# Kernel tuning notes

Hardware: AMD Instinct MI355X
Metric: run time of the kernel (lower is better)

The kernel has to match this reference:

```python
import jax, jax.numpy as jnp
import numpy as np

B, T, F = 256, 2000, 42
H_VAD, H_NOISE, H_DEN = 24, 48, 96

def _gru_params(key, in_dim, hid):
    k1, k2, k3, k4 = jax.random.split(key, 4)
    s = 1.0 / np.sqrt(hid)
    return (jax.random.uniform(k1, (3 * hid, in_dim), jnp.float32, -s, s),
            jax.random.uniform(k2, (3 * hid, hid), jnp.float32, -s, s),
            jax.random.uniform(k3, (3 * hid,), jnp.float32, -s, s),
            jax.random.uniform(k4, (3 * hid,), jnp.float32, -s, s))

def setup_inputs() -> dict:
    key = jax.random.key(0)
    ks = jax.random.split(key, 12)
    x = jax.random.normal(ks[0], (B, T, F), jnp.float32)
    sd = 1.0 / np.sqrt(F)
    dense_w = jax.random.uniform(ks[1], (24, F), jnp.float32, -sd, sd)
    dense_b = jax.random.uniform(ks[2], (24,), jnp.float32, -sd, sd)
    vad_w_ih, vad_w_hh, vad_b_ih, vad_b_hh = _gru_params(ks[3], 24, H_VAD)
    sv = 1.0 / np.sqrt(H_VAD)
    vad_out_w = jax.random.uniform(ks[4], (1, H_VAD), jnp.float32, -sv, sv)
    vad_out_b = jax.random.uniform(ks[5], (1,), jnp.float32, -sv, sv)
    noise_w_ih, noise_w_hh, noise_b_ih, noise_b_hh = _gru_params(ks[6], F + 24 + H_VAD, H_NOISE)
    den_w_ih, den_w_hh, den_b_ih, den_b_hh = _gru_params(ks[7], F + H_VAD + H_NOISE, H_DEN)
    so = 1.0 / np.sqrt(H_DEN)
    out_w = jax.random.uniform(ks[8], (22, H_DEN), jnp.float32, -so, so)
    out_b = jax.random.uniform(ks[9], (22,), jnp.float32, -so, so)
    return dict(x=x, dense_w=dense_w, dense_b=dense_b,
                vad_w_ih=vad_w_ih, vad_w_hh=vad_w_hh, vad_b_ih=vad_b_ih, vad_b_hh=vad_b_hh,
                vad_out_w=vad_out_w, vad_out_b=vad_out_b,
                noise_w_ih=noise_w_ih, noise_w_hh=noise_w_hh, noise_b_ih=noise_b_ih, noise_b_hh=noise_b_hh,
                den_w_ih=den_w_ih, den_w_hh=den_w_hh, den_b_ih=den_b_ih, den_b_hh=den_b_hh,
                out_w=out_w, out_b=out_b)

def _gru(x_seq, w_ih, w_hh, b_ih, b_hh):
    # PyTorch GRU semantics, batch_first. x_seq: [B,T,I] -> hidden seq [B,T,H]
    hid = w_hh.shape[1]
    gx = jnp.einsum('bti,gi->btg', x_seq, w_ih) + b_ih  # precompute input gates [B,T,3H]
    h0 = jnp.zeros((x_seq.shape[0], hid), x_seq.dtype)
    def step(h, gx_t):
        gh = h @ w_hh.T + b_hh
        xr, xz, xn = jnp.split(gx_t, 3, axis=-1)
        hr, hz, hn = jnp.split(gh, 3, axis=-1)
        r = jax.nn.sigmoid(xr + hr)
        z = jax.nn.sigmoid(xz + hz)
        n = jnp.tanh(xn + r * hn)
        h_new = (1.0 - z) * n + z * h
        return h_new, h_new
    _, hs = jax.lax.scan(step, h0, jnp.swapaxes(gx, 0, 1))  # hs: [T,B,H]
    return jnp.swapaxes(hs, 0, 1)

def reference(x, dense_w, dense_b, vad_w_ih, vad_w_hh, vad_b_ih, vad_b_hh,
              vad_out_w, vad_out_b, noise_w_ih, noise_w_hh, noise_b_ih, noise_b_hh,
              den_w_ih, den_w_hh, den_b_ih, den_b_hh, out_w, out_b):
    tmp = jnp.tanh(jnp.einsum('btf,of->bto', x, dense_w) + dense_b)
    vad_gru = _gru(tmp, vad_w_ih, vad_w_hh, vad_b_ih, vad_b_hh)
    vad_out = jax.nn.sigmoid(jnp.einsum('bth,oh->bto', vad_gru, vad_out_w) + vad_out_b)
    noise_in = jnp.concatenate([tmp, vad_gru, x], axis=-1)
    noise_gru = _gru(noise_in, noise_w_ih, noise_w_hh, noise_b_ih, noise_b_hh)
    den_in = jnp.concatenate([vad_gru, jax.nn.relu(noise_gru), x], axis=-1)
    den_gru = _gru(den_in, den_w_ih, den_w_hh, den_b_ih, den_b_hh)
    den_out = jax.nn.sigmoid(jnp.einsum('bth,oh->bto', jax.nn.relu(den_gru), out_w) + out_b)
    return (den_out, vad_out)
```

## Files before the change

### kernel.cpp

```cpp
#include <hip/hip_runtime.h>
#include <hip/hip_bf16.h>

#define BB 256
#define TT 2000
#define FF 42
#define NTHREADS 640

__device__ __forceinline__ float bf2f(__hip_bfloat16 v) { return __bfloat162float(v); }
__device__ __forceinline__ float sig(float x) { return 1.0f / (1.0f + __expf(-x)); }
__device__ __forceinline__ float tanh_fast(float x) {
    float e = __expf(2.0f * x);
    return 1.0f - 2.0f / (e + 1.0f);
}
__device__ __forceinline__ float unpk_lo(unsigned u) {
    union { unsigned u; float f; } c; c.u = u << 16; return c.f;
}
__device__ __forceinline__ float unpk_hi(unsigned u) {
    union { unsigned u; float f; } c; c.u = u & 0xffff0000u; return c.f;
}
__device__ __forceinline__ unsigned f2bfbits(float f) {
    union { float f; unsigned u; } c; c.f = f;
    unsigned r = c.u + 0x7FFFu + ((c.u >> 16) & 1u);
    return r >> 16;
}
__device__ __forceinline__ unsigned pack2(float a, float b) {
    return f2bfbits(a) | (f2bfbits(b) << 16);
}
__device__ __forceinline__ float gld(const void* p, int i, bool f32) {
    return f32 ? ((const float*)p)[i] : bf2f(((const __hip_bfloat16*)p)[i]);
}

template<int NW>
__device__ __forceinline__ float dot_w2(const unsigned* __restrict__ w,
                                        const float* __restrict__ in, float acc) {
    const float2* in2 = (const float2*)in;
    float a0 = acc, a1 = 0.f;
    #pragma unroll
    for (int i = 0; i < NW; ++i) {
        unsigned u = w[i];
        float2 d = in2[i];
        a0 = fmaf(unpk_lo(u), d.x, a0);
        a1 = fmaf(unpk_hi(u), d.y, a1);
    }
    return a0 + a1;
}
template<int NW>
__device__ __forceinline__ float dot_reg2(const unsigned (&w)[57],
                                          const float* __restrict__ in, float acc) {
    const float2* in2 = (const float2*)in;
    float a0 = acc, a1 = 0.f;
    #pragma unroll
    for (int i = 0; i < NW; ++i) {
        unsigned u = w[i];
        float2 d = in2[i];
        a0 = fmaf(unpk_lo(u), d.x, a0);
        a1 = fmaf(unpk_hi(u), d.y, a1);
    }
    return a0 + a1;
}

__device__ void load_rows(unsigned* dst, const void* src, int O, int Kw, int K, int S,
                          int tid, int nt, bool f32) {
    for (int i = tid; i < O * Kw; i += nt) {
        int o = i / Kw, kp = i - o * Kw;
        dst[o * S + kp] = pack2(gld(src, o * K + 2 * kp, f32),
                                gld(src, o * K + 2 * kp + 1, f32));
    }
}
__device__ void load_V(float* dst, const void* src, int n, int tid, int nt, bool f32) {
    for (int i = tid; i < n; i += nt) dst[i] = gld(src, i, f32);
}

__global__ __launch_bounds__(NTHREADS, 1)
void rnn_fused(const void* __restrict__ x,
               const void* __restrict__ dense_w, const void* __restrict__ dense_b,
               const void* __restrict__ vad_w_ih, const void* __restrict__ vad_w_hh,
               const void* __restrict__ vad_b_ih, const void* __restrict__ vad_b_hh,
               const void* __restrict__ vad_out_w, const void* __restrict__ vad_out_b,
               const void* __restrict__ noise_w_ih, const void* __restrict__ noise_w_hh,
               const void* __restrict__ noise_b_ih, const void* __restrict__ noise_b_hh,
               const void* __restrict__ den_w_ih, const void* __restrict__ den_w_hh,
               const void* __restrict__ den_b_ih, const void* __restrict__ den_b_hh,
               const void* __restrict__ out_w, const void* __restrict__ out_b,
               void* __restrict__ d_out) {
    __shared__ __align__(16) unsigned sDWp[24 * 21];
    __shared__ __align__(16) unsigned sVIHp[72 * 13];
    __shared__ __align__(16) unsigned sVHHp[72 * 13];
    __shared__ __align__(16) unsigned sNIHp[144 * 45];
    __shared__ __align__(16) unsigned sNHHp[144 * 25];
    __shared__ __align__(16) unsigned sOWp[22 * 49];
    __shared__ unsigned sVOWp[12];
    __shared__ float sDB[24], sVBI[72], sVBH[72], sNBI[144], sNBH[144], sOB[22], sVOB[1];
    __shared__ __align__(16) float sXT[44];
    __shared__ __align__(16) float sTMP[24];
    __shared__ __align__(16) float sHV[24];
    __shared__ __align__(16) float sHN[48];
    __shared__ __align__(16) float sHD[96];
    __shared__ __align__(16) float sHR[96];
    __shared__ __align__(16) float sNIN[92];
    __shared__ __align__(16) float sDIN[116];
    __shared__ float sVPI[72], sVPH[72];
    __shared__ float sNPI[144], sNPH[144];
    __shared__ float sGI[288], sGH[288];
    __shared__ int sBad;

    const int tid = threadIdx.x;
    const int b = blockIdx.x;
    const int nt = NTHREADS;

    if (tid == 0) sBad = 0;
    __syncthreads();
    {
        const unsigned* w = (const unsigned*)dense_w;
        for (int i = tid; i < 500; i += nt) {
            float av = fabsf(unpk_lo(w[i]));
            if (!(av <= 1e3f)) { atomicAdd(&sBad, 1); break; }
        }
    }
    __syncthreads();
    const bool F32 = (sBad > 0);

    const float* xbf = (const float*)x + (size_t)b * TT * FF;
    const __hip_bfloat16* xbh = (const __hip_bfloat16*)x + (size_t)b * TT * FF;
    float* odf = (float*)d_out;
    __hip_bfloat16* odh = (__hip_bfloat16*)d_out;
    float* ovf = odf + (size_t)BB * TT * 22;
    __hip_bfloat16* ovh = odh + (size_t)BB * TT * 22;

    load_rows(sDWp,  dense_w,    24, 21, 42, 21, tid, nt, F32);
    load_rows(sVIHp, vad_w_ih,   72, 12, 24, 13, tid, nt, F32);
    load_rows(sVHHp, vad_w_hh,   72, 12, 24, 13, tid, nt, F32);
    load_rows(sNIHp, noise_w_ih, 144, 45, 90, 45, tid, nt, F32);
    load_rows(sNHHp, noise_w_hh, 144, 24, 48, 25, tid, nt, F32);
    load_rows(sOWp,  out_w,      22, 48, 96, 49, tid, nt, F32);
    if (tid < 12) sVOWp[tid] = pack2(gld(vad_out_w, 2 * tid, F32),
                                     gld(vad_out_w, 2 * tid + 1, F32));
    load_V(sDB,  dense_b,    24, tid, nt, F32);
    load_V(sVBI, vad_b_ih,   72, tid, nt, F32);
    load_V(sVBH, vad_b_hh,   72, tid, nt, F32);
    load_V(sNBI, noise_b_ih, 144, tid, nt, F32);
    load_V(sNBH, noise_b_hh, 144, tid, nt, F32);
    load_V(sOB,  out_b,      22, tid, nt, F32);
    if (tid == 0) sVOB[0] = gld(vad_out_b, 0, F32);

    unsigned wden[57];
    float bDen = 0.f;
    if (tid < 288) {
        #pragma unroll
        for (int i = 0; i < 57; ++i)
            wden[i] = pack2(gld(den_w_ih, tid * 114 + 2 * i, F32),
                            gld(den_w_ih, tid * 114 + 2 * i + 1, F32));
        bDen = gld(den_b_ih, tid, F32);
    } else if (tid >= 320 && tid < 608) {
        int o = tid - 320;
        #pragma unroll
        for (int i = 0; i < 48; ++i)
            wden[i] = pack2(gld(den_w_hh, o * 96 + 2 * i, F32),
                            gld(den_w_hh, o * 96 + 2 * i + 1, F32));
        #pragma unroll
        for (int i = 48; i < 57; ++i) wden[i] = 0u;
        bDen = gld(den_b_hh, o, F32);
    } else {
        #pragma unroll
        for (int i = 0; i < 57; ++i) wden[i] = 0u;
    }

    for (int i = tid; i < 24; i += nt) { sHV[i] = 0.f; sTMP[i] = 0.f; }
    for (int i = tid; i < 48; i += nt) sHN[i] = 0.f;
    for (int i = tid; i < 96; i += nt) { sHD[i] = 0.f; sHR[i] = 0.f; }
    if (tid < 2) { sXT[42 + tid] = 0.f; sNIN[90 + tid] = 0.f; sDIN[114 + tid] = 0.f; }
    float xreg = 0.f;
    if (tid >= 128 && tid < 128 + FF) {
        int j = tid - 128;
        float v = F32 ? xbf[j] : bf2f(xbh[j]);
        sXT[j] = v;
        sNIN[48 + j] = v;
        sDIN[72 + j] = v;
        xreg = F32 ? xbf[FF + j] : bf2f(xbh[FF + j]);
    }
    __syncthreads();

    for (int t = 0; t < TT; ++t) {
        if (tid < 24) {
            float v = tanh_fast(dot_w2<21>(sDWp + tid * 21, sXT, sDB[tid]));
            sTMP[tid] = v;
            sNIN[tid] = v;
        } else if (tid >= 64 && tid < 86) {
            if (t > 0) {
                int o = tid - 64;
                float a = dot_w2<48>(sOWp + o * 49, sHR, sOB[o]);
                size_t oi = ((size_t)b * TT + (t - 1)) * 22 + o;
                float v = sig(a);
                if (F32) odf[oi] = v; else odh[oi] = __float2bfloat16(v);
            }
        }
        __syncthreads();

        if (tid < 72) {
            sVPI[tid] = dot_w2<12>(sVIHp + tid * 13, sTMP, sVBI[tid]);
        } else if (tid >= 128 && tid < 200) {
            int o = tid - 128;
            sVPH[o] = dot_w2<12>(sVHHp + o * 13, sHV, sVBH[o]);
        }
        __syncthreads();

        if (tid < 24) {
            float r = sig(sVPI[tid] + sVPH[tid]);
            float z = sig(sVPI[24 + tid] + sVPH[24 + tid]);
            float n = tanh_fast(sVPI[48 + tid] + r * sVPH[48 + tid]);
            float h = (1.f - z) * n + z * sHV[tid];
            sHV[tid] = h;
            sNIN[24 + tid] = h;
            sDIN[tid] = h;
        }
        __syncthreads();

        if (tid < 144) {
            sNPI[tid] = dot_w2<45>(sNIHp + tid * 45, sNIN, sNBI[tid]);
        } else if (tid >= 192 && tid < 336) {
            int o = tid - 192;
            sNPH[o] = dot_w2<24>(sNHHp + o * 25, sHN, sNBH[o]);
        }
        __syncthreads();

        if (tid < 48) {
            float r = sig(sNPI[tid] + sNPH[tid]);
            float z = sig(sNPI[48 + tid] + sNPH[48 + tid]);
            float n = tanh_fast(sNPI[96 + tid] + r * sNPH[96 + tid]);
            float h = (1.f - z) * n + z * sHN[tid];
            sHN[tid] = h;
            sDIN[24 + tid] = fmaxf(h, 0.f);
        }
        __syncthreads();

        if (tid < 288) {
            sGI[tid] = dot_reg2<57>(wden, sDIN, bDen);
        } else if (tid >= 320 && tid < 608) {
            sGH[tid - 320] = dot_reg2<48>(wden, sHD, bDen);
        }
        __syncthreads();

        if (tid < 96) {
            float r = sig(sGI[tid] + sGH[tid]);
            float z = sig(sGI[96 + tid] + sGH[96 + tid]);
            float n = tanh_fast(sGI[192 + tid] + r * sGH[192 + tid]);
            float h = (1.f - z) * n + z * sHD[tid];
            sHD[tid] = h;
            sHR[tid] = fmaxf(h, 0.f);
        } else if (tid >= 128 && tid < 128 + FF) {
            if (t + 1 < TT) {
                int j = tid - 128;
                sXT[j] = xreg;
                sNIN[48 + j] = xreg;
                sDIN[72 + j] = xreg;
                int t2 = (t + 2 < TT) ? (t + 2) : (TT - 1);
                xreg = F32 ? xbf[t2 * FF + j] : bf2f(xbh[t2 * FF + j]);
            }
        } else if (tid == 200) {
            float a = sVOB[0];
            const float2* hv2 = (const float2*)sHV;
            #pragma unroll
            for (int i = 0; i < 12; ++i) {
                unsigned u = sVOWp[i];
                float2 d = hv2[i];
                a = fmaf(unpk_lo(u), d.x, a);
                a = fmaf(unpk_hi(u), d.y, a);
            }
            size_t oi = (size_t)b * TT + t;
            float v = sig(a);
            if (F32) ovf[oi] = v; else ovh[oi] = __float2bfloat16(v);
        }
        __syncthreads();
    }

    if (tid >= 64 && tid < 86) {
        int o = tid - 64;
        float a = dot_w2<48>(sOWp + o * 49, sHR, sOB[o]);
        size_t oi = ((size_t)b * TT + (TT - 1)) * 22 + o;
        float v = sig(a);
        if (F32) odf[oi] = v; else odh[oi] = __float2bfloat16(v);
    }
}

extern "C" void kernel_launch(void* const* d_in, const int* in_sizes, int n_in,
                              void* d_out, int out_size, void* d_ws, size_t ws_size,
                              hipStream_t stream) {
    hipLaunchKernelGGL(rnn_fused, dim3(BB), dim3(NTHREADS), 0, stream,
                       d_in[0], d_in[1], d_in[2],
                       d_in[3], d_in[4], d_in[5], d_in[6],
                       d_in[7], d_in[8],
                       d_in[9], d_in[10], d_in[11], d_in[12],
                       d_in[13], d_in[14], d_in[15], d_in[16],
                       d_in[17], d_in[18], d_out);
}
```

Before: 10.04 ms.

## Restructure per-step schedule to cut barriers and overlap GRU stages

Reorganizes the per-timestep pipeline. The VAD GRU is fused into one 24-thread stage that computes all six gate dots and the update without a separate barrier. The dense-layer tanh for the next step and the den hidden-hidden matvec are moved into earlier stages so they overlap other work, and biases are held in registers instead of shared memory. The goal is fewer __syncthreads per step along the sequential critical path. In exchange, each VAD thread now does six dot products serially, and the x-staging logic is more intricate, so there is a risk of ordering bugs.

```diff
diff --git a/kernel.cpp b/kernel.cpp
--- a/kernel.cpp
+++ b/kernel.cpp
@@ -29,6 +29,7 @@
 __device__ __forceinline__ float gld(const void* p, int i, bool f32) {
     return f32 ? ((const float*)p)[i] : bf2f(((const __hip_bfloat16*)p)[i]);
 }
+
 
 template<int NW>
 __device__ __forceinline__ float dot_w2(const unsigned* __restrict__ w,
@@ -66,9 +67,6 @@
         dst[o * S + kp] = pack2(gld(src, o * K + 2 * kp, f32),
                                 gld(src, o * K + 2 * kp + 1, f32));
     }
-}
-__device__ void load_V(float* dst, const void* src, int n, int tid, int nt, bool f32) {
-    for (int i = tid; i < n; i += nt) dst[i] = gld(src, i, f32);
 }
 
 __global__ __launch_bounds__(NTHREADS, 1)
@@ -90,7 +88,6 @@
     __shared__ __align__(16) unsigned sNHHp[144 * 25];
     __shared__ __align__(16) unsigned sOWp[22 * 49];
     __shared__ unsigned sVOWp[12];
-    __shared__ float sDB[24], sVBI[72], sVBH[72], sNBI[144], sNBH[144], sOB[22], sVOB[1];
     __shared__ __align__(16) float sXT[44];
     __shared__ __align__(16) float sTMP[24];
     __shared__ __align__(16) float sHV[24];
@@ -99,7 +96,6 @@
     __shared__ __align__(16) float sHR[96];
     __shared__ __align__(16) float sNIN[92];
     __shared__ __align__(16) float sDIN[116];
-    __shared__ float sVPI[72], sVPH[72];
     __shared__ float sNPI[144], sNPH[144];
     __shared__ float sGI[288], sGH[288];
     __shared__ int sBad;
@@ -135,13 +131,6 @@
     load_rows(sOWp,  out_w,      22, 48, 96, 49, tid, nt, F32);
     if (tid < 12) sVOWp[tid] = pack2(gld(vad_out_w, 2 * tid, F32),
                                      gld(vad_out_w, 2 * tid + 1, F32));
-    load_V(sDB,  dense_b,    24, tid, nt, F32);
-    load_V(sVBI, vad_b_ih,   72, tid, nt, F32);
-    load_V(sVBH, vad_b_hh,   72, tid, nt, F32);
-    load_V(sNBI, noise_b_ih, 144, tid, nt, F32);
-    load_V(sNBH, noise_b_hh, 144, tid, nt, F32);
-    load_V(sOB,  out_b,      22, tid, nt, F32);
-    if (tid == 0) sVOB[0] = gld(vad_out_b, 0, F32);
 
     unsigned wden[57];
     float bDen = 0.f;
@@ -165,61 +154,79 @@
         for (int i = 0; i < 57; ++i) wden[i] = 0u;
     }
 
+    float bDn = 0.f, bNI = 0.f, bNH = 0.f, bOut = 0.f, bVo = 0.f;
+    float bv0 = 0.f, bv1 = 0.f, bv2 = 0.f, bv3 = 0.f, bv4 = 0.f, bv5 = 0.f;
+    float hvreg = 0.f;
+    if (tid >= 96 && tid < 120) bDn = gld(dense_b, tid - 96, F32);
+    if (tid >= 288 && tid < 312) {
+        int o = tid - 288;
+        bv0 = gld(vad_b_ih, o, F32);      bv1 = gld(vad_b_ih, 24 + o, F32);
+        bv2 = gld(vad_b_ih, 48 + o, F32); bv3 = gld(vad_b_hh, o, F32);
+        bv4 = gld(vad_b_hh, 24 + o, F32); bv5 = gld(vad_b_hh, 48 + o, F32);
+    }
+    if (tid == 312) bVo = gld(vad_out_b, 0, F32);
+    if (tid >= 320 && tid < 464) bNI = gld(noise_b_ih, tid - 320, F32);
+    if (tid >= 464 && tid < 608) bNH = gld(noise_b_hh, tid - 464, F32);
+    if (tid >= 608 && tid < 630) bOut = gld(out_b, tid - 608, F32);
+
     for (int i = tid; i < 24; i += nt) { sHV[i] = 0.f; sTMP[i] = 0.f; }
     for (int i = tid; i < 48; i += nt) sHN[i] = 0.f;
     for (int i = tid; i < 96; i += nt) { sHD[i] = 0.f; sHR[i] = 0.f; }
     if (tid < 2) { sXT[42 + tid] = 0.f; sNIN[90 + tid] = 0.f; sDIN[114 + tid] = 0.f; }
+    if (tid < FF) {
+        float v = F32 ? xbf[tid] : bf2f(xbh[tid]);
+        sXT[tid] = v; sNIN[48 + tid] = v; sDIN[72 + tid] = v;
+    }
     float xreg = 0.f;
-    if (tid >= 128 && tid < 128 + FF) {
-        int j = tid - 128;
-        float v = F32 ? xbf[j] : bf2f(xbh[j]);
-        sXT[j] = v;
-        sNIN[48 + j] = v;
-        sDIN[72 + j] = v;
+    if (tid >= 464 && tid < 464 + FF) {
+        int j = tid - 464;
         xreg = F32 ? xbf[FF + j] : bf2f(xbh[FF + j]);
     }
     __syncthreads();
+    if (tid >= 96 && tid < 120) {
+        int o = tid - 96;
+        float v = tanh_fast(dot_w2<21>(sDWp + o * 21, sXT, bDn));
+        sTMP[o] = v; sNIN[o] = v;
+    }
+    __syncthreads();
 
     for (int t = 0; t < TT; ++t) {
-        if (tid < 24) {
-            float v = tanh_fast(dot_w2<21>(sDWp + tid * 21, sXT, sDB[tid]));
-            sTMP[tid] = v;
-            sNIN[tid] = v;
-        } else if (tid >= 64 && tid < 86) {
+        if (tid >= 320 && tid < 608) {
+            sGH[tid - 320] = dot_reg2<48>(wden, sHD, bDen);
+        } else if (tid >= 288 && tid < 312) {
+            int o = tid - 288;
+            const unsigned* wi = sVIHp + o * 13;
+            const unsigned* wh = sVHHp + o * 13;
+            float xr = dot_w2<12>(wi,       sTMP, bv0);
+            float xz = dot_w2<12>(wi + 312, sTMP, bv1);
+            float xn = dot_w2<12>(wi + 624, sTMP, bv2);
+            float hr = dot_w2<12>(wh,       sHV, bv3);
+            float hz = dot_w2<12>(wh + 312, sHV, bv4);
+            float hn = dot_w2<12>(wh + 624, sHV, bv5);
+            float r = sig(xr + hr);
+            float z = sig(xz + hz);
+            float n = tanh_fast(xn + r * hn);
+            float h = (1.f - z) * n + z * hvreg;
+            hvreg = h;
+            sHV[o] = h; sNIN[24 + o] = h; sDIN[o] = h;
+        } else if (tid >= 608 && tid < 630) {
             if (t > 0) {
-                int o = tid - 64;
-                float a = dot_w2<48>(sOWp + o * 49, sHR, sOB[o]);
+                int o = tid - 608;
+                float v = sig(dot_w2<48>(sOWp + o * 49, sHR, bOut));
                 size_t oi = ((size_t)b * TT + (t - 1)) * 22 + o;
-                float v = sig(a);
                 if (F32) odf[oi] = v; else odh[oi] = __float2bfloat16(v);
             }
         }
         __syncthreads();
 
-        if (tid < 72) {
-            sVPI[tid] = dot_w2<12>(sVIHp + tid * 13, sTMP, sVBI[tid]);
-        } else if (tid >= 128 && tid < 200) {
-            int o = tid - 128;
-            sVPH[o] = dot_w2<12>(sVHHp + o * 13, sHV, sVBH[o]);
-        }
-        __syncthreads();
-
-        if (tid < 24) {
-            float r = sig(sVPI[tid] + sVPH[tid]);
-            float z = sig(sVPI[24 + tid] + sVPH[24 + tid]);
-            float n = tanh_fast(sVPI[48 + tid] + r * sVPH[48 + tid]);
-            float h = (1.f - z) * n + z * sHV[tid];
-            sHV[tid] = h;
-            sNIN[24 + tid] = h;
-            sDIN[tid] = h;
-        }
-        __syncthreads();
-
-        if (tid < 144) {
-            sNPI[tid] = dot_w2<45>(sNIHp + tid * 45, sNIN, sNBI[tid]);
-        } else if (tid >= 192 && tid < 336) {
-            int o = tid - 192;
-            sNPH[o] = dot_w2<24>(sNHHp + o * 25, sHN, sNBH[o]);
+        if (tid >= 320 && tid < 464) {
+            sNPI[tid - 320] = dot_w2<45>(sNIHp + (tid - 320) * 45, sNIN, bNI);
+        } else if (tid >= 464 && tid < 608) {
+            sNPH[tid - 464] = dot_w2<24>(sNHHp + (tid - 464) * 25, sHN, bNH);
+        } else if (tid == 312) {
+            float v = sig(dot_w2<12>(sVOWp, sHV, bVo));
+            size_t oi = (size_t)b * TT + t;
+            if (F32) ovf[oi] = v; else ovh[oi] = __float2bfloat16(v);
         }
         __syncthreads();
 
@@ -235,8 +242,11 @@
 
         if (tid < 288) {
             sGI[tid] = dot_reg2<57>(wden, sDIN, bDen);
-        } else if (tid >= 320 && tid < 608) {
-            sGH[tid - 320] = dot_reg2<48>(wden, sHD, bDen);
+        } else if (tid >= 464 && tid < 464 + FF) {
+            int j = tid - 464;
+            sXT[j] = xreg; sNIN[48 + j] = xreg;
+            int t2 = (t + 2 < TT) ? (t + 2) : (TT - 1);
+            xreg = F32 ? xbf[t2 * FF + j] : bf2f(xbh[t2 * FF + j]);
         }
         __syncthreads();
 
@@ -247,37 +257,21 @@
             float h = (1.f - z) * n + z * sHD[tid];
             sHD[tid] = h;
             sHR[tid] = fmaxf(h, 0.f);
+        } else if (tid < 120) {
+            int o = tid - 96;
+            float v = tanh_fast(dot_w2<21>(sDWp + o * 21, sXT, bDn));
+            sTMP[o] = v; sNIN[o] = v;
         } else if (tid >= 128 && tid < 128 + FF) {
-            if (t + 1 < TT) {
-                int j = tid - 128;
-                sXT[j] = xreg;
-                sNIN[48 + j] = xreg;
-                sDIN[72 + j] = xreg;
-                int t2 = (t + 2 < TT) ? (t + 2) : (TT - 1);
-                xreg = F32 ? xbf[t2 * FF + j] : bf2f(xbh[t2 * FF + j]);
-            }
-        } else if (tid == 200) {
-            float a = sVOB[0];
-            const float2* hv2 = (const float2*)sHV;
-            #pragma unroll
-            for (int i = 0; i < 12; ++i) {
-                unsigned u = sVOWp[i];
-                float2 d = hv2[i];
-                a = fmaf(unpk_lo(u), d.x, a);
-                a = fmaf(unpk_hi(u), d.y, a);
-            }
-            size_t oi = (size_t)b * TT + t;
-            float v = sig(a);
-            if (F32) ovf[oi] = v; else ovh[oi] = __float2bfloat16(v);
-        }
-        __syncthreads();
-    }
-
-    if (tid >= 64 && tid < 86) {
-        int o = tid - 64;
-        float a = dot_w2<48>(sOWp + o * 49, sHR, sOB[o]);
+            int j = tid - 128;
+            sDIN[72 + j] = sXT[j];
+        }
+        __syncthreads();
+    }
+
+    if (tid >= 608 && tid < 630) {
+        int o = tid - 608;
+        float v = sig(dot_w2<48>(sOWp + o * 49, sHR, bOut));
         size_t oi = ((size_t)b * TT + (TT - 1)) * 22 + o;
-        float v = sig(a);
         if (F32) odf[oi] = v; else odh[oi] = __float2bfloat16(v);
     }
 }
```

After: 13.11 ms. 30.5% more time.
